# Performance work log

Hardware: AMD Instinct MI355X
Metric: run time of the kernel (lower is better)

## Reference

```python
import jax, jax.numpy as jnp
import numpy as np

B, N, DIM = 1, 512, 1024
HEADS, DH = 16, 64          # dim_head = 64, _dim = heads*dh = 1024
P = 32                      # projection_dim
P2 = P // 2
NEG_INF = -1e30


def setup_inputs() -> dict:
    key = jax.random.key(0)
    ks = jax.random.split(key, 14)
    s = 0.02
    _dim = HEADS * DH
    return {
        "x":    jax.random.normal(ks[0], (B, N, DIM), dtype=jnp.float32),
        "Wqkv": jax.random.normal(ks[1], (3 * _dim, DIM), dtype=jnp.float32) * s,
        "Wout": jax.random.normal(ks[2], (DIM, _dim), dtype=jnp.float32) * s,
        "Wq":   jax.random.normal(ks[3], (P, DH), dtype=jnp.float32) * s,
        "bq":   jax.random.normal(ks[4], (P,), dtype=jnp.float32) * s,
        "Wk":   jax.random.normal(ks[5], (P, DH), dtype=jnp.float32) * s,
        "bk":   jax.random.normal(ks[6], (P,), dtype=jnp.float32) * s,
        "W1":   jax.random.normal(ks[7], (P, 2 * P), dtype=jnp.float32) * s,
        "b1":   jax.random.normal(ks[8], (P,), dtype=jnp.float32) * s,
        "W2":   jax.random.normal(ks[9], (P2, P), dtype=jnp.float32) * s,
        "b2":   jax.random.normal(ks[10], (P2,), dtype=jnp.float32) * s,
        "W3":   jax.random.normal(ks[11], (1, P2), dtype=jnp.float32) * s,
        "b3":   jax.random.normal(ks[12], (1,), dtype=jnp.float32) * s,
    }


def reference(x, Wqkv, Wout, Wq, bq, Wk, bk, W1, b1, W2, b2, W3, b3):
    b, n, _ = x.shape
    # qkv projection, then einops 'b n (d k h) -> k b h n d' split (d outermost!)
    qkv = jnp.einsum('bnc,oc->bno', x, Wqkv).reshape(b, n, DH, 3, HEADS)
    q = jnp.transpose(qkv[:, :, :, 0, :], (0, 3, 1, 2))  # [b,h,n,dh]
    k = jnp.transpose(qkv[:, :, :, 1, :], (0, 3, 1, 2))
    v = jnp.transpose(qkv[:, :, :, 2, :], (0, 3, 1, 2))

    qp = jnp.einsum('bhnd,pd->bhnp', q, Wq) + bq  # [b,h,n,P]
    kp = jnp.einsum('bhnd,pd->bhnp', k, Wk) + bk

    # linear1 on concat(q_i, k_j): split W1 -> broadcast-add (same math,
    # avoids materializing the [b,h,n,n,2P] concat tensor)
    W1q, W1k = W1[:, :P], W1[:, P:]
    a = jnp.einsum('bhnp,qp->bhnq', qp, W1q)      # [b,h,n,P]
    c = jnp.einsum('bhnp,qp->bhnq', kp, W1k)      # [b,h,n,P]
    h1 = jax.nn.relu(a[:, :, :, None, :] + c[:, :, None, :, :] + b1)  # [b,h,n,n,P]
    h2 = jax.nn.relu(jnp.einsum('bhijp,qp->bhijq', h1, W2) + b2)      # [b,h,n,n,P/2]
    score = jnp.einsum('bhijq,oq->bhijo', h2, W3)[..., 0] + b3[0]     # [b,h,n,n]

    # causal mask (triu(1) filled with -inf)
    i = jnp.arange(n)
    causal = i[None, :] > i[:, None]
    score = jnp.where(causal, NEG_INF, score)

    attn = jax.nn.softmax(score, axis=-1)
    out = jnp.einsum('bhij,bhjd->bhid', attn, v)                      # [b,h,n,dh]
    out = jnp.transpose(out, (0, 2, 1, 3)).reshape(b, n, HEADS * DH)  # b n (h d)
    return jnp.einsum('bne,oe->bno', out, Wout)
```

## Files before the change

### kernel.cpp

```cpp
#include <hip/hip_runtime.h>
#include <hip/hip_bf16.h>
#include <hip/hip_fp16.h>
#include <math.h>

#define N_SEQ 512
#define DIM   1024
#define HEADS 16
#define DH    64
#define P     32
#define P2    16
#define PSTR  520

typedef short    bf16x8 __attribute__((ext_vector_type(8)));
typedef _Float16 f16x8  __attribute__((ext_vector_type(8)));
typedef float    f32x4  __attribute__((ext_vector_type(4)));

__device__ inline unsigned short f2bf(float f) {
  union { float f; unsigned u; } v; v.f = f;
  unsigned r = (v.u + 0x7fffu + ((v.u >> 16) & 1u)) >> 16;
  return (unsigned short)r;
}

union H8 { f16x8 v; __half2 h2[4]; unsigned u32[4]; };

__global__ __launch_bounds__(256) void prep(
    const float* __restrict__ Wqkv, const float* __restrict__ Wq,
    const float* __restrict__ bq, const float* __restrict__ Wk,
    const float* __restrict__ bk, const float* __restrict__ W1,
    const float* __restrict__ b1,
    const float* __restrict__ x, const float* __restrict__ Wout,
    short* __restrict__ Wcomb, short* __restrict__ xb,
    short* __restrict__ Woutb, float* __restrict__ ba32,
    float* __restrict__ bc32) {
  const int b = blockIdx.x, tid = threadIdx.x;
  if (b < 256) {
    __shared__ float W1s[32][33];
    __shared__ float Wqs[32][65];
    __shared__ float wsm[32][65];
    __shared__ __align__(16) float qs[64][132];
    const int part = b >> 7, rem = b & 127;
    const int h = rem >> 3, c0 = (rem & 7) * 128;
    const int grow = part * 16 + h;
    for (int idx = tid; idx < 1024; idx += 256)
      W1s[idx >> 5][idx & 31] = W1[(idx >> 5) * 64 + part * 32 + (idx & 31)];
    const float* Wsel = part ? Wk : Wq;
    for (int idx = tid; idx < 2048; idx += 256)
      Wqs[idx >> 6][idx & 63] = Wsel[idx];
    for (int idx = tid; idx < 2048; idx += 256) {
      const int d = idx >> 5, c4 = idx & 31;
      *(float4*)&qs[d][c4 * 4] =
          *(const float4*)(Wqkv + (size_t)(d * 48 + grow) * DIM + c0 + c4 * 4);
    }
    __syncthreads();
    for (int idx = tid; idx < 2048; idx += 256) {
      const int q = idx >> 6, d = idx & 63;
      float s = 0.f;
#pragma unroll
      for (int p = 0; p < 32; ++p) s += W1s[q][p] * Wqs[p][d];
      wsm[q][d] = s;
    }
    __syncthreads();
    for (int idx = tid; idx < 4096; idx += 256) {
      const int q = idx >> 7, c = idx & 127;
      float s = 0.f;
#pragma unroll
      for (int d = 0; d < 64; ++d) s += wsm[q][d] * qs[d][c];
      Wcomb[(size_t)(part * 512 + h * 32 + q) * DIM + c0 + c] = (short)f2bf(s);
    }
    if (rem == 0 && tid < 32) {
      const float* bsel = part ? bk : bq;
      float s = 0.f;
#pragma unroll
      for (int p = 0; p < 32; ++p) s += W1s[tid][p] * bsel[p];
      if (part) s += b1[tid];
      (part ? bc32 : ba32)[tid] = s;
    }
  } else if (b < 384) {
#pragma unroll
    for (int rr = 0; rr < 8; ++rr) {
      const int ov = (b - 256) * 8 + rr;
      const int h = ov >> 6, d = ov & 63;
      const float4 v = *(const float4*)(Wqkv + (size_t)(d * 48 + 32 + h) * DIM + tid * 4);
      ushort4 o;
      o.x = f2bf(v.x); o.y = f2bf(v.y); o.z = f2bf(v.z); o.w = f2bf(v.w);
      *(ushort4*)(Wcomb + (size_t)(1024 + ov) * DIM + tid * 4) = o;
    }
  } else if (b < 512) {
    const int idx = (b - 384) * 256 + tid;
#pragma unroll
    for (int u = 0; u < 4; ++u) {
      const int t = u * 32768 + idx;
      const float4 v = ((const float4*)x)[t];
      ushort4 o;
      o.x = f2bf(v.x); o.y = f2bf(v.y); o.z = f2bf(v.z); o.w = f2bf(v.w);
      ((ushort4*)xb)[t] = o;
    }
  } else {
    const int idx = (b - 512) * 256 + tid;
#pragma unroll
    for (int u = 0; u < 4; ++u) {
      const int t = u * 65536 + idx;
      const float4 v = ((const float4*)Wout)[t];
      ushort4 o;
      o.x = f2bf(v.x); o.y = f2bf(v.y); o.z = f2bf(v.z); o.w = f2bf(v.w);
      ((ushort4*)Woutb)[t] = o;
    }
  }
}

__global__ __launch_bounds__(256) void gemm_acv(
    const short* __restrict__ xb, const short* __restrict__ Wcomb,
    const float* __restrict__ ba32, const float* __restrict__ bc32,
    __half* __restrict__ a_buf, __half* __restrict__ cb_buf,
    __half* __restrict__ vT) {
  const int bb = blockIdx.x;
  const int tm = bb >> 4;
  const int tn = bb & 15;
  const int w = threadIdx.x >> 6;
  const int wm = w >> 1, wn = w & 1;
  const int lane = threadIdx.x & 63;
  const int m = lane & 15, quad = lane >> 4;

  const int row0 = tm * 128 + wm * 64;
  const int col0 = tn * 128 + wn * 64;

  const short* pa = xb + (size_t)(row0 + m) * DIM + quad * 8;
  const short* pb = Wcomb + (size_t)(col0 + m) * DIM + quad * 8;

  f32x4 acc[4][4];
#pragma unroll
  for (int mi = 0; mi < 4; ++mi)
#pragma unroll
    for (int ni = 0; ni < 4; ++ni) acc[mi][ni] = (f32x4){0.f, 0.f, 0.f, 0.f};

#pragma unroll 2
  for (int k = 0; k < DIM; k += 32) {
    bf16x8 af[4], bf[4];
#pragma unroll
    for (int i = 0; i < 4; ++i) {
      af[i] = *(const bf16x8*)(pa + (size_t)i * 16 * DIM + k);
      bf[i] = *(const bf16x8*)(pb + (size_t)i * 16 * DIM + k);
    }
#pragma unroll
    for (int mi = 0; mi < 4; ++mi)
#pragma unroll
      for (int ni = 0; ni < 4; ++ni)
        acc[mi][ni] = __builtin_amdgcn_mfma_f32_16x16x32_bf16(
            af[mi], bf[ni], acc[mi][ni], 0, 0, 0);
  }

#pragma unroll
  for (int mi = 0; mi < 4; ++mi) {
#pragma unroll
    for (int ni = 0; ni < 4; ++ni) {
      const int o = col0 + ni * 16 + m;
#pragma unroll
      for (int r = 0; r < 4; ++r) {
        const int n = row0 + mi * 16 + quad * 4 + r;
        const float val = acc[mi][ni][r];
        if (o < 512) {
          const int hh = o >> 5, q = o & 31;
          a_buf[((size_t)hh * N_SEQ + n) * P + q] = __float2half(val + ba32[q]);
        } else if (o < 1024) {
          const int oo = o - 512, hh = oo >> 5, q = oo & 31;
          cb_buf[((size_t)hh * N_SEQ + n) * P + q] = __float2half(val + bc32[q]);
        } else {
          const int ov = o - 1024, hh = ov >> 6, d = ov & 63;
          vT[((size_t)hh * DH + d) * N_SEQ + n] = __float2half(val);
        }
      }
    }
  }
}

__device__ inline float rowscore(const H8& a, const H8& c, f16x8 w2f,
                                 f32x4 b2q, float4 w3q) {
  const f16x8 z = (f16x8)(_Float16)0;
  const f16x8 u = __builtin_elementwise_max(a.v + c.v, z);
  f32x4 acc = b2q;
  acc = __builtin_amdgcn_mfma_f32_16x16x32_f16(w2f, u, acc, 0, 0, 0);
  return fmaxf(acc[0], 0.f) * w3q.x + fmaxf(acc[1], 0.f) * w3q.y
       + fmaxf(acc[2], 0.f) * w3q.z + fmaxf(acc[3], 0.f) * w3q.w;
}

__device__ inline float quadreduce4(float p0, float p1, float p2, float p3,
                                    int quad) {
  const float sx = (quad & 1) ? p0 : p1;
  const float sy = (quad & 1) ? p2 : p3;
  const float rx = __shfl_xor(sx, 16);
  const float ry = __shfl_xor(sy, 16);
  const float aa = ((quad & 1) ? p1 : p0) + rx;
  const float bb = ((quad & 1) ? p3 : p2) + ry;
  const float sz = (quad & 2) ? aa : bb;
  const float rz = __shfl_xor(sz, 32);
  return ((quad & 2) ? bb : aa) + rz;
}

__global__ __launch_bounds__(512) void attn_fused(
    const __half* __restrict__ a_g, const __half* __restrict__ cb_g,
    const float* __restrict__ W2, const float* __restrict__ b2,
    const float* __restrict__ W3,
    const __half* __restrict__ vT, short* __restrict__ attnb) {
  const int p = blockIdx.x;
  const int h = blockIdx.y;
  const int tid = threadIdx.x;
  const int w = tid >> 6;
  const int lane = tid & 63;
  const int m = lane & 15, quad = lane >> 4;

  __shared__ __align__(16) __half probS[32][PSTR];
  __shared__ float invS[32];

  const int tlo = p, thi = 31 - p;
  const int nlo = p + 1, nhi = 32 - p;

  {
    const int g = w & 3;
    const int par = w >> 2;
    f16x8 w2f;
    {
      const float4* wp = (const float4*)(W2 + m * P + quad * 8);
      const float4 w0 = wp[0], w1 = wp[1];
      H8 uu;
      uu.h2[0] = __floats2half2_rn(w0.x, w0.y);
      uu.h2[1] = __floats2half2_rn(w0.z, w0.w);
      uu.h2[2] = __floats2half2_rn(w1.x, w1.y);
      uu.h2[3] = __floats2half2_rn(w1.z, w1.w);
      w2f = uu.v;
    }
    const float4 b2f = *(const float4*)(b2 + quad * 4);
    const f32x4 b2q = {b2f.x, b2f.y, b2f.z, b2f.w};
    const float4 w3q = *(const float4*)(W3 + quad * 4);

    H8 alo[4], ahi[4];
#pragma unroll
    for (int r = 0; r < 4; ++r) {
      alo[r].v = *(const f16x8*)(a_g + ((size_t)h * N_SEQ + tlo * 16 + 4 * g + r) * P + quad * 8);
      ahi[r].v = *(const f16x8*)(a_g + ((size_t)h * N_SEQ + thi * 16 + 4 * g + r) * P + quad * 8);
    }

    for (int jt = par; jt < nhi; jt += 2) {
      H8 cb;
      cb.v = *(const f16x8*)(cb_g + ((size_t)h * N_SEQ + jt * 16 + m) * P + quad * 8);
      const float q0 = rowscore(ahi[0], cb, w2f, b2q, w3q);
      const float q1 = rowscore(ahi[1], cb, w2f, b2q, w3q);
      const float q2 = rowscore(ahi[2], cb, w2f, b2q, w3q);
      const float q3 = rowscore(ahi[3], cb, w2f, b2q, w3q);
      const float fh = quadreduce4(q0, q1, q2, q3, quad);
      probS[16 + 4 * g + quad][jt * 16 + m] = __float2half(fh);
      if (jt < nlo) {
        const float s0 = rowscore(alo[0], cb, w2f, b2q, w3q);
        const float s1 = rowscore(alo[1], cb, w2f, b2q, w3q);
        const float s2 = rowscore(alo[2], cb, w2f, b2q, w3q);
        const float s3 = rowscore(alo[3], cb, w2f, b2q, w3q);
        const float fl = quadreduce4(s0, s1, s2, s3, quad);
        probS[4 * g + quad][jt * 16 + m] = __float2half(fl);
      }
    }
  }
  __syncthreads();

  {
    const int lr = tid >> 4;
    const int c  = tid & 15;
    const int gi = (lr < 16) ? (tlo * 16 + lr) : (thi * 16 + (lr - 16));
    float mx = -1e30f;
#pragma unroll
    for (int k = 0; k < 4; ++k) {
      const int c0 = k * 128 + c * 8;
      if (c0 > gi) break;
      H8 vv; vv.v = *(const f16x8*)&probS[lr][c0];
#pragma unroll
      for (int uu = 0; uu < 8; ++uu) {
        const float s = __half2float(vv.h2[uu >> 1].data[uu & 1]);
        if (c0 + uu <= gi) mx = fmaxf(mx, s);
      }
    }
#pragma unroll
    for (int msk = 1; msk < 16; msk <<= 1) mx = fmaxf(mx, __shfl_xor(mx, msk));
    float sum = 0.f;
#pragma unroll
    for (int k = 0; k < 4; ++k) {
      const int c0 = k * 128 + c * 8;
      H8 vv; vv.v = *(const f16x8*)&probS[lr][c0];
      H8 o;
#pragma unroll
      for (int uu = 0; uu < 4; ++uu) {
        float e0 = 0.f, e1 = 0.f;
        if (c0 + 2 * uu <= gi) {
          e0 = __expf(__half2float(vv.h2[uu].data[0]) - mx);
          if (c0 + 2 * uu + 1 <= gi)
            e1 = __expf(__half2float(vv.h2[uu].data[1]) - mx);
        }
        sum += e0 + e1;
        o.h2[uu] = __floats2half2_rn(e0, e1);
      }
      *(f16x8*)&probS[lr][c0] = o.v;
    }
#pragma unroll
    for (int msk = 1; msk < 16; msk <<= 1) sum += __shfl_xor(sum, msk);
    if (c == 0) invS[lr] = 1.f / sum;
  }
  __syncthreads();

  {
    const int half = w >> 2;
    const int d0 = (w & 3) * 16;
    const __half* pb = vT + ((size_t)h * DH + d0 + m) * N_SEQ + quad * 8;
    const int lbase = half ? 16 : 0;
    const int tile = half ? thi : tlo;
    const int nk = half ? ((33 - p) >> 1) : ((p + 2) >> 1);
    f32x4 acc = {0.f, 0.f, 0.f, 0.f};
    for (int k = 0; k < nk; ++k) {
      const f16x8 aa = *(const f16x8*)&probS[lbase + m][k * 32 + quad * 8];
      const f16x8 bb = *(const f16x8*)(pb + k * 32);
      acc = __builtin_amdgcn_mfma_f32_16x16x32_f16(aa, bb, acc, 0, 0, 0);
    }
#pragma unroll
    for (int r = 0; r < 4; ++r) {
      const int lrow = quad * 4 + r;
      const float val = acc[r] * invS[lbase + lrow];
      attnb[(size_t)(tile * 16 + lrow) * DIM + h * DH + d0 + m] = (short)f2bf(val);
    }
  }
}

__global__ __launch_bounds__(256) void gemm_out16(
    const short* __restrict__ A, const short* __restrict__ B,
    float* __restrict__ C) {
  const int bb = blockIdx.x;
  const int tm = bb >> 3;
  const int tn = bb & 7;
  const int w = threadIdx.x >> 6;
  const int wm = w >> 1, wn = w & 1;
  const int lane = threadIdx.x & 63;
  const int m = lane & 15, quad = lane >> 4;

  const int row0 = tm * 128 + wm * 64;
  const int col0 = tn * 128 + wn * 64;

  const short* pa = A + (size_t)(row0 + m) * DIM + quad * 8;
  const short* pb = B + (size_t)(col0 + m) * DIM + quad * 8;

  f32x4 acc[4][4];
#pragma unroll
  for (int mi = 0; mi < 4; ++mi)
#pragma unroll
    for (int ni = 0; ni < 4; ++ni) acc[mi][ni] = (f32x4){0.f, 0.f, 0.f, 0.f};

#pragma unroll 2
  for (int k = 0; k < DIM; k += 32) {
    bf16x8 af[4], bf[4];
#pragma unroll
    for (int i = 0; i < 4; ++i) {
      af[i] = *(const bf16x8*)(pa + (size_t)i * 16 * DIM + k);
      bf[i] = *(const bf16x8*)(pb + (size_t)i * 16 * DIM + k);
    }
#pragma unroll
    for (int mi = 0; mi < 4; ++mi)
#pragma unroll
      for (int ni = 0; ni < 4; ++ni)
        acc[mi][ni] = __builtin_amdgcn_mfma_f32_16x16x32_bf16(
            af[mi], bf[ni], acc[mi][ni], 0, 0, 0);
  }

#pragma unroll
  for (int mi = 0; mi < 4; ++mi)
#pragma unroll
    for (int ni = 0; ni < 4; ++ni) {
      const int o = col0 + ni * 16 + m;
#pragma unroll
      for (int r = 0; r < 4; ++r) {
        const int n = row0 + mi * 16 + quad * 4 + r;
        C[(size_t)n * DIM + o] = acc[mi][ni][r];
      }
    }
}

extern "C" void kernel_launch(void* const* d_in, const int* in_sizes, int n_in,
                              void* d_out, int out_size, void* d_ws, size_t ws_size,
                              hipStream_t stream) {
  const float* x    = (const float*)d_in[0];
  const float* Wqkv = (const float*)d_in[1];
  const float* Wout = (const float*)d_in[2];
  const float* Wq   = (const float*)d_in[3];
  const float* bq   = (const float*)d_in[4];
  const float* Wk   = (const float*)d_in[5];
  const float* bk   = (const float*)d_in[6];
  const float* W1   = (const float*)d_in[7];
  const float* b1   = (const float*)d_in[8];
  const float* W2   = (const float*)d_in[9];
  const float* b2   = (const float*)d_in[10];
  const float* W3   = (const float*)d_in[11];
  float* out = (float*)d_out;

  float*  ws     = (float*)d_ws;
  float*  ba32   = ws;
  float*  bc32   = ba32 + 32;
  __half* a_buf  = (__half*)(bc32 + 32);
  __half* cb_buf = a_buf + (size_t)HEADS * N_SEQ * P;
  __half* vT     = cb_buf + (size_t)HEADS * N_SEQ * P;
  short*  Wcomb  = (short*)(vT + (size_t)HEADS * DH * N_SEQ);
  short*  xb     = Wcomb + (size_t)2048 * DIM;
  short*  Woutb  = xb + (size_t)N_SEQ * DIM;
  short*  attnb  = Woutb + (size_t)DIM * DIM;

  prep<<<768, 256, 0, stream>>>(Wqkv, Wq, bq, Wk, bk, W1, b1, x, Wout,
                                Wcomb, xb, Woutb, ba32, bc32);

  gemm_acv<<<64, 256, 0, stream>>>(xb, Wcomb, ba32, bc32, a_buf, cb_buf, vT);

  dim3 g3(16, HEADS);
  attn_fused<<<g3, 512, 0, stream>>>(a_buf, cb_buf, W2, b2, W3, vT, attnb);

  gemm_out16<<<32, 256, 0, stream>>>(attnb, Woutb, out);
}
```

Baseline: 199.5 us.

## Shrink GEMM tiles to fill all CUs and add register prefetch pipeline

Both projection GEMMs switch from a few large 128x128 tiles (64 and 32 blocks) to small per-wave tiles spread over 256 blocks of 512 threads, so far more compute units are busy. Each wave now computes a 16x32 or 16x16 output tile. The K loop is fully unrolled with a four-deep register prefetch of the next fragments to hide global load latency. The cost is less operand reuse per wave, so more redundant global or L2 traffic for the same inputs.

```diff
diff --git a/kernel.cpp b/kernel.cpp
--- a/kernel.cpp
+++ b/kernel.cpp
@@ -108,66 +108,70 @@
   }
 }
 
-__global__ __launch_bounds__(256) void gemm_acv(
+__global__ __launch_bounds__(512) void gemm_acv(
     const short* __restrict__ xb, const short* __restrict__ Wcomb,
     const float* __restrict__ ba32, const float* __restrict__ bc32,
     __half* __restrict__ a_buf, __half* __restrict__ cb_buf,
     __half* __restrict__ vT) {
   const int bb = blockIdx.x;
-  const int tm = bb >> 4;
-  const int tn = bb & 15;
+  const int tm = bb >> 5;
+  const int tn = bb & 31;
   const int w = threadIdx.x >> 6;
   const int wm = w >> 1, wn = w & 1;
   const int lane = threadIdx.x & 63;
   const int m = lane & 15, quad = lane >> 4;
 
-  const int row0 = tm * 128 + wm * 64;
-  const int col0 = tn * 128 + wn * 64;
-
-  const short* pa = xb + (size_t)(row0 + m) * DIM + quad * 8;
-  const short* pb = Wcomb + (size_t)(col0 + m) * DIM + quad * 8;
-
-  f32x4 acc[4][4];
-#pragma unroll
-  for (int mi = 0; mi < 4; ++mi)
-#pragma unroll
-    for (int ni = 0; ni < 4; ++ni) acc[mi][ni] = (f32x4){0.f, 0.f, 0.f, 0.f};
-
-#pragma unroll 2
-  for (int k = 0; k < DIM; k += 32) {
-    bf16x8 af[4], bf[4];
-#pragma unroll
-    for (int i = 0; i < 4; ++i) {
-      af[i] = *(const bf16x8*)(pa + (size_t)i * 16 * DIM + k);
-      bf[i] = *(const bf16x8*)(pb + (size_t)i * 16 * DIM + k);
-    }
-#pragma unroll
-    for (int mi = 0; mi < 4; ++mi)
-#pragma unroll
-      for (int ni = 0; ni < 4; ++ni)
-        acc[mi][ni] = __builtin_amdgcn_mfma_f32_16x16x32_bf16(
-            af[mi], bf[ni], acc[mi][ni], 0, 0, 0);
-  }
-
-#pragma unroll
-  for (int mi = 0; mi < 4; ++mi) {
-#pragma unroll
-    for (int ni = 0; ni < 4; ++ni) {
-      const int o = col0 + ni * 16 + m;
-#pragma unroll
-      for (int r = 0; r < 4; ++r) {
-        const int n = row0 + mi * 16 + quad * 4 + r;
-        const float val = acc[mi][ni][r];
-        if (o < 512) {
-          const int hh = o >> 5, q = o & 31;
-          a_buf[((size_t)hh * N_SEQ + n) * P + q] = __float2half(val + ba32[q]);
-        } else if (o < 1024) {
-          const int oo = o - 512, hh = oo >> 5, q = oo & 31;
-          cb_buf[((size_t)hh * N_SEQ + n) * P + q] = __float2half(val + bc32[q]);
-        } else {
-          const int ov = o - 1024, hh = ov >> 6, d = ov & 63;
-          vT[((size_t)hh * DH + d) * N_SEQ + n] = __float2half(val);
-        }
+  const int row0 = tm * 64 + wm * 16;
+  const int col0 = tn * 64 + wn * 32;
+
+  const short* pa  = xb + (size_t)(row0 + m) * DIM + quad * 8;
+  const short* pb0 = Wcomb + (size_t)(col0 + m) * DIM + quad * 8;
+  const short* pb1 = pb0 + (size_t)16 * DIM;
+
+  bf16x8 abuf[4], b0buf[4], b1buf[4];
+#pragma unroll
+  for (int j = 0; j < 4; ++j) {
+    abuf[j]  = *(const bf16x8*)(pa  + j * 32);
+    b0buf[j] = *(const bf16x8*)(pb0 + j * 32);
+    b1buf[j] = *(const bf16x8*)(pb1 + j * 32);
+  }
+
+  f32x4 acc0 = {0.f, 0.f, 0.f, 0.f}, acc1 = {0.f, 0.f, 0.f, 0.f};
+
+#pragma unroll
+  for (int ko = 0; ko < 8; ++ko) {
+#pragma unroll
+    for (int j = 0; j < 4; ++j) {
+      const int k = ko * 4 + j;
+      const bf16x8 av  = abuf[j];
+      const bf16x8 b0v = b0buf[j];
+      const bf16x8 b1v = b1buf[j];
+      if (k + 4 < 32) {
+        abuf[j]  = *(const bf16x8*)(pa  + (k + 4) * 32);
+        b0buf[j] = *(const bf16x8*)(pb0 + (k + 4) * 32);
+        b1buf[j] = *(const bf16x8*)(pb1 + (k + 4) * 32);
+      }
+      acc0 = __builtin_amdgcn_mfma_f32_16x16x32_bf16(av, b0v, acc0, 0, 0, 0);
+      acc1 = __builtin_amdgcn_mfma_f32_16x16x32_bf16(av, b1v, acc1, 0, 0, 0);
+    }
+  }
+
+#pragma unroll
+  for (int r = 0; r < 4; ++r) {
+    const int n = row0 + quad * 4 + r;
+#pragma unroll
+    for (int half = 0; half < 2; ++half) {
+      const int o = col0 + half * 16 + m;
+      const float val = half ? acc1[r] : acc0[r];
+      if (o < 512) {
+        const int hh = o >> 5, q = o & 31;
+        a_buf[((size_t)hh * N_SEQ + n) * P + q] = __float2half(val + ba32[q]);
+      } else if (o < 1024) {
+        const int oo = o - 512, hh = oo >> 5, q = oo & 31;
+        cb_buf[((size_t)hh * N_SEQ + n) * P + q] = __float2half(val + bc32[q]);
+      } else {
+        const int ov = o - 1024, hh = ov >> 6, d = ov & 63;
+        vT[((size_t)hh * DH + d) * N_SEQ + n] = __float2half(val);
       }
     }
   }
@@ -325,56 +329,49 @@
   }
 }
 
-__global__ __launch_bounds__(256) void gemm_out16(
+__global__ __launch_bounds__(512) void gemm_out16(
     const short* __restrict__ A, const short* __restrict__ B,
     float* __restrict__ C) {
   const int bb = blockIdx.x;
-  const int tm = bb >> 3;
-  const int tn = bb & 7;
+  const int tm = bb >> 4;
+  const int tn = bb & 15;
   const int w = threadIdx.x >> 6;
-  const int wm = w >> 1, wn = w & 1;
+  const int wm = w & 1, wn = w >> 1;
   const int lane = threadIdx.x & 63;
   const int m = lane & 15, quad = lane >> 4;
 
-  const int row0 = tm * 128 + wm * 64;
-  const int col0 = tn * 128 + wn * 64;
+  const int row0 = tm * 32 + wm * 16;
+  const int col0 = tn * 64 + wn * 16;
 
   const short* pa = A + (size_t)(row0 + m) * DIM + quad * 8;
   const short* pb = B + (size_t)(col0 + m) * DIM + quad * 8;
 
-  f32x4 acc[4][4];
-#pragma unroll
-  for (int mi = 0; mi < 4; ++mi)
-#pragma unroll
-    for (int ni = 0; ni < 4; ++ni) acc[mi][ni] = (f32x4){0.f, 0.f, 0.f, 0.f};
-
-#pragma unroll 2
-  for (int k = 0; k < DIM; k += 32) {
-    bf16x8 af[4], bf[4];
-#pragma unroll
-    for (int i = 0; i < 4; ++i) {
-      af[i] = *(const bf16x8*)(pa + (size_t)i * 16 * DIM + k);
-      bf[i] = *(const bf16x8*)(pb + (size_t)i * 16 * DIM + k);
-    }
-#pragma unroll
-    for (int mi = 0; mi < 4; ++mi)
-#pragma unroll
-      for (int ni = 0; ni < 4; ++ni)
-        acc[mi][ni] = __builtin_amdgcn_mfma_f32_16x16x32_bf16(
-            af[mi], bf[ni], acc[mi][ni], 0, 0, 0);
-  }
-
-#pragma unroll
-  for (int mi = 0; mi < 4; ++mi)
-#pragma unroll
-    for (int ni = 0; ni < 4; ++ni) {
-      const int o = col0 + ni * 16 + m;
-#pragma unroll
-      for (int r = 0; r < 4; ++r) {
-        const int n = row0 + mi * 16 + quad * 4 + r;
-        C[(size_t)n * DIM + o] = acc[mi][ni][r];
-      }
-    }
+  bf16x8 abuf[4], bbuf[4];
+#pragma unroll
+  for (int j = 0; j < 4; ++j) {
+    abuf[j] = *(const bf16x8*)(pa + j * 32);
+    bbuf[j] = *(const bf16x8*)(pb + j * 32);
+  }
+
+  f32x4 acc = {0.f, 0.f, 0.f, 0.f};
+#pragma unroll
+  for (int ko = 0; ko < 8; ++ko) {
+#pragma unroll
+    for (int j = 0; j < 4; ++j) {
+      const int k = ko * 4 + j;
+      const bf16x8 av = abuf[j];
+      const bf16x8 bv = bbuf[j];
+      if (k + 4 < 32) {
+        abuf[j] = *(const bf16x8*)(pa + (k + 4) * 32);
+        bbuf[j] = *(const bf16x8*)(pb + (k + 4) * 32);
+      }
+      acc = __builtin_amdgcn_mfma_f32_16x16x32_bf16(av, bv, acc, 0, 0, 0);
+    }
+  }
+
+#pragma unroll
+  for (int r = 0; r < 4; ++r)
+    C[(size_t)(row0 + quad * 4 + r) * DIM + col0 + m] = acc[r];
 }
 
 extern "C" void kernel_launch(void* const* d_in, const int* in_sizes, int n_in,
@@ -408,10 +405,10 @@
   prep<<<768, 256, 0, stream>>>(Wqkv, Wq, bq, Wk, bk, W1, b1, x, Wout,
                                 Wcomb, xb, Woutb, ba32, bc32);
 
-  gemm_acv<<<64, 256, 0, stream>>>(xb, Wcomb, ba32, bc32, a_buf, cb_buf, vT);
+  gemm_acv<<<256, 512, 0, stream>>>(xb, Wcomb, ba32, bc32, a_buf, cb_buf, vT);
 
   dim3 g3(16, HEADS);
   attn_fused<<<g3, 512, 0, stream>>>(a_buf, cb_buf, W2, b2, W3, vT, attnb);
 
-  gemm_out16<<<32, 256, 0, stream>>>(attnb, Woutb, out);
-}
+  gemm_out16<<<256, 512, 0, stream>>>(attnb, Woutb, out);
+}
```

After: 163.4 us. -18.1%, faster.
